# Kernel optimization log

Hardware: AMD Instinct MI355X
Metric: run time of the kernel (lower is better)

Reference implementation:

```python
import jax, jax.numpy as jnp
import numpy as np

# ---- module constants (from init_kwargs) ----
EMBED_DIM = 384
NUM_HYPEREDGES = 128
TOPK = 64
SPATIAL_SHAPE = (16, 32, 32)  # D, H, W -> N = 16384
SPACING = (2.0, 1.0, 1.0)
SPATIAL_WEIGHT = 0.1
B, N, C = 4, 16 * 32 * 32, EMBED_DIM


def _l2norm(x, axis=-1, eps=1e-12):
    n = jnp.linalg.norm(x, axis=axis, keepdims=True)
    return x / jnp.maximum(n, eps)


def _get_3d_coords():
    D, H, W = SPATIAL_SHAPE
    z = jnp.arange(D, dtype=jnp.float32) * SPACING[0]
    y = jnp.arange(H, dtype=jnp.float32) * SPACING[1]
    x = jnp.arange(W, dtype=jnp.float32) * SPACING[2]
    zz, yy, xx = jnp.meshgrid(z, y, x, indexing='ij')
    return jnp.stack([zz, yy, xx], axis=-1).reshape(-1, 3)  # (N, 3)


def setup_inputs() -> dict:
    key = jax.random.key(0)
    k1, k2 = jax.random.split(key)
    node_features = jax.random.normal(k1, (B, N, C), dtype=jnp.float32)
    class_token = jax.random.normal(k2, (1, 1, C), dtype=jnp.float32)
    temperature = jnp.ones((1,), dtype=jnp.float32) * 0.07
    return {"node_features": node_features, "class_token": class_token, "temperature": temperature}


def reference(node_features, class_token, temperature):
    Ne = NUM_HYPEREDGES
    w = SPATIAL_WEIGHT
    temp = temperature[0]

    nodes_n = _l2norm(node_features)                      # (B, N, C)

    # Step 1: center sampling by semantic similarity to class token
    ct_n = _l2norm(jnp.broadcast_to(class_token, (B, 1, C)))
    scores = jnp.einsum('boc,bnc->bn', ct_n, nodes_n) / temp  # (B, N)
    _, center_idx = jax.lax.top_k(scores, Ne)             # (B, Ne)

    # Gather centers and compute cosine sim of every center vs all nodes
    centers = jnp.take_along_axis(node_features, center_idx[:, :, None], axis=1)  # (B, Ne, C)
    centers_n = _l2norm(centers)
    sem_sim = jnp.einsum('bec,bnc->ben', centers_n, nodes_n) / temp  # (B, Ne, N)

    # Spatial bias (normalized distance from each center voxel)
    coords = _get_3d_coords()                             # (N, 3)
    center_coords = coords[center_idx]                    # (B, Ne, 3)
    diff = coords[None, None, :, :] - center_coords[:, :, None, :]  # (B, Ne, N, 3)
    dist = jnp.linalg.norm(diff, axis=-1)                 # (B, Ne, N)
    dist = dist / (jnp.max(dist, axis=-1, keepdims=True) + 1e-8)
    combined = (1.0 - w) * sem_sim + w * (1.0 - dist)     # (B, Ne, N)

    # Per-hyperedge top-K neighbors -> incidence matrix H (B, N, Ne)
    _, nbr_idx = jax.lax.top_k(combined, TOPK)            # (B, Ne, K)
    b_ix = jnp.arange(B)[:, None, None]
    e_ix = jnp.arange(Ne)[None, :, None]
    Hmat = jnp.zeros((B, N, Ne), dtype=node_features.dtype)
    Hmat = Hmat.at[b_ix, nbr_idx, e_ix].set(1.0)
    return Hmat
```

## Files before the change

### kernel.cpp

```cpp
#include <hip/hip_runtime.h>
#include <math.h>

#define BB 4
#define NN 16384
#define CC 384
#define NE 128
#define KK 64
#define CAP 1024

typedef unsigned short ushort_t;
typedef __attribute__((ext_vector_type(8))) short bf16x8;
typedef __attribute__((ext_vector_type(4))) float f32x4;
#define MFMA(a, b, c) __builtin_amdgcn_mfma_f32_16x16x32_bf16(a, b, c, 0, 0, 0)

__device__ inline unsigned fkey(float f) {
    unsigned b = __float_as_uint(f);
    return (b & 0x80000000u) ? ~b : (b | 0x80000000u);
}
__device__ inline ushort_t bf16rne(float f) {
    unsigned u = __float_as_uint(f);
    unsigned r = u + 0x7FFFu + ((u >> 16) & 1u);
    return (ushort_t)(r >> 16);
}
__device__ inline float bf16tof(ushort_t h) {
    return __uint_as_float(((unsigned)h) << 16);
}
__device__ inline void cvt2(float fa, float fb, unsigned& hp, unsigned& lp) {
    unsigned ua = __float_as_uint(fa), ub = __float_as_uint(fb);
    unsigned ra = ua + 0x8000u, rb = ub + 0x8000u;
    hp = (ra >> 16) | (rb & 0xFFFF0000u);
    float ha = __uint_as_float(ra & 0xFFFF0000u);
    float hb = __uint_as_float(rb & 0xFFFF0000u);
    float la = fa - ha, lb = fb - hb;
    unsigned lra = __float_as_uint(la) + 0x8000u;
    unsigned lrb = __float_as_uint(lb) + 0x8000u;
    lp = (lra >> 16) | (lrb & 0xFFFF0000u);
}

__device__ inline void bin_select4k(const unsigned* hist, int t, int* wsum,
                                    int* sh_bin, int* sh_r, int r) {
    int base = t * 4;
    int c0 = hist[base], c1 = hist[base + 1], c2 = hist[base + 2], c3 = hist[base + 3];
    int csum = c0 + c1 + c2 + c3;
    int lane = t & 63, wid = t >> 6;
    int x = csum;
#pragma unroll
    for (int off = 1; off < 64; off <<= 1) {
        int v = __shfl_down(x, off, 64);
        if (lane + off < 64) x += v;
    }
    if (lane == 0) wsum[wid] = x;
    __syncthreads();
    int after = 0;
    for (int w2 = wid + 1; w2 < 16; ++w2) after += wsum[w2];
    int S = x - csum + after;
    if (S < r && S + c3 >= r) { *sh_bin = base + 3; *sh_r = r - S; }
    S += c3;
    if (S < r && S + c2 >= r) { *sh_bin = base + 2; *sh_r = r - S; }
    S += c2;
    if (S < r && S + c1 >= r) { *sh_bin = base + 1; *sh_r = r - S; }
    S += c1;
    if (S < r && S + c0 >= r) { *sh_bin = base + 0; *sh_r = r - S; }
    __syncthreads();
}

__global__ __launch_bounds__(256) void k_scores(const float* __restrict__ nf,
                                                const float* __restrict__ ct,
                                                unsigned* __restrict__ keys,
                                                float* __restrict__ invn) {
    int wave = threadIdx.x >> 6;
    int lane = threadIdx.x & 63;
    int row  = blockIdx.x * 4 + wave;
    const float* x = nf + (size_t)row * CC;
    float4 a  = ((const float4*)x)[lane];
    float2 c2 = ((const float2*)(x + 256))[lane];
    float4 ta = ((const float4*)ct)[lane];
    float2 tc = ((const float2*)(ct + 256))[lane];
    float ss = a.x*a.x + a.y*a.y + a.z*a.z + a.w*a.w + c2.x*c2.x + c2.y*c2.y;
    float dt = ta.x*a.x + ta.y*a.y + ta.z*a.z + ta.w*a.w + tc.x*c2.x + tc.y*c2.y;
#pragma unroll
    for (int off = 32; off; off >>= 1) {
        ss += __shfl_xor(ss, off, 64);
        dt += __shfl_xor(dt, off, 64);
    }
    if (lane == 0) {
        float inv = 1.0f / fmaxf(sqrtf(ss), 1e-12f);
        invn[row] = inv;
        keys[row] = fkey(dt * inv);
    }
}

__global__ __launch_bounds__(1024) void k_top128(const unsigned* __restrict__ keys,
                                                 const float* __restrict__ nf,
                                                 const float* __restrict__ invn,
                                                 ushort_t* __restrict__ Ahi,
                                                 ushort_t* __restrict__ Alo,
                                                 float* __restrict__ meta) {
    __shared__ unsigned hist[4096];
    __shared__ int wsum[16];
    __shared__ int sh_bin, sh_r;
    __shared__ unsigned cu[NE];
    __shared__ int cil[NE];
    __shared__ unsigned eqk[CAP];
    __shared__ int eqi[CAP];
    __shared__ int cnt_gt, cnt_eq;
    __shared__ int ocid[NE];
    int b = blockIdx.x;
    int t = threadIdx.x;
    const uint4* rowv = (const uint4*)(keys + b * NN);
    if (t == 0) { cnt_gt = 0; cnt_eq = 0; }
    ((uint4*)hist)[t] = make_uint4(0, 0, 0, 0);
    __syncthreads();
    uint4 u0 = rowv[t], u1 = rowv[t + 1024], u2 = rowv[t + 2048], u3 = rowv[t + 3072];
    atomicAdd(&hist[u0.x >> 20], 1u); atomicAdd(&hist[u0.y >> 20], 1u);
    atomicAdd(&hist[u0.z >> 20], 1u); atomicAdd(&hist[u0.w >> 20], 1u);
    atomicAdd(&hist[u1.x >> 20], 1u); atomicAdd(&hist[u1.y >> 20], 1u);
    atomicAdd(&hist[u1.z >> 20], 1u); atomicAdd(&hist[u1.w >> 20], 1u);
    atomicAdd(&hist[u2.x >> 20], 1u); atomicAdd(&hist[u2.y >> 20], 1u);
    atomicAdd(&hist[u2.z >> 20], 1u); atomicAdd(&hist[u2.w >> 20], 1u);
    atomicAdd(&hist[u3.x >> 20], 1u); atomicAdd(&hist[u3.y >> 20], 1u);
    atomicAdd(&hist[u3.z >> 20], 1u); atomicAdd(&hist[u3.w >> 20], 1u);
    __syncthreads();
    bin_select4k(hist, t, wsum, &sh_bin, &sh_r, NE);
    unsigned bin = (unsigned)sh_bin;
    int r = sh_r;
#define EMIT128(uu, nn) { unsigned tb = (uu) >> 20; \
    if (tb > bin) { int p = atomicAdd(&cnt_gt, 1); cu[p] = (uu); cil[p] = (nn); } \
    else if (tb == bin) { int p = atomicAdd(&cnt_eq, 1); if (p < CAP) { eqk[p] = (uu); eqi[p] = (nn); } } }
    EMIT128(u0.x, 4*t+0); EMIT128(u0.y, 4*t+1); EMIT128(u0.z, 4*t+2); EMIT128(u0.w, 4*t+3);
    EMIT128(u1.x, 4096+4*t+0); EMIT128(u1.y, 4096+4*t+1); EMIT128(u1.z, 4096+4*t+2); EMIT128(u1.w, 4096+4*t+3);
    EMIT128(u2.x, 8192+4*t+0); EMIT128(u2.y, 8192+4*t+1); EMIT128(u2.z, 8192+4*t+2); EMIT128(u2.w, 8192+4*t+3);
    EMIT128(u3.x, 12288+4*t+0); EMIT128(u3.y, 12288+4*t+1); EMIT128(u3.z, 12288+4*t+2); EMIT128(u3.w, 12288+4*t+3);
#undef EMIT128
    __syncthreads();
    int ne = cnt_eq < CAP ? cnt_eq : CAP;
    for (int i = t; i < ne; i += 1024) {
        unsigned ki = eqk[i]; int ii = eqi[i], rk = 0;
        for (int j = 0; j < ne; ++j) {
            unsigned kj = eqk[j];
            rk += (kj > ki) || (kj == ki && eqi[j] < ii);
        }
        if (rk < r) { cu[cnt_gt + rk] = ki; cil[cnt_gt + rk] = ii; }
    }
    __syncthreads();
    if (t < NE) {
        unsigned mu = cu[t]; int mi = cil[t], rk = 0;
#pragma unroll 4
        for (int j = 0; j < NE; ++j) {
            unsigned ou = cu[j]; int oi = cil[j];
            rk += (ou > mu) || (ou == mu && oi < mi);
        }
        ocid[rk] = mi;
    }
    __syncthreads();
    {
        int e = t >> 3, part = t & 7;
        int ci = ocid[e];
        float inv = invn[b * NN + ci];
        const float4* src = (const float4*)(nf + ((size_t)b * NN + ci) * CC) + part * 12;
        ushort_t* dh = Ahi + ((size_t)b * NE + e) * CC + part * 48;
        ushort_t* dl = Alo + ((size_t)b * NE + e) * CC + part * 48;
#pragma unroll
        for (int i = 0; i < 12; ++i) {
            float4 f = src[i];
            f.x *= inv; f.y *= inv; f.z *= inv; f.w *= inv;
            ushort4 h, l;
            h.x = bf16rne(f.x); l.x = bf16rne(f.x - bf16tof(h.x));
            h.y = bf16rne(f.y); l.y = bf16rne(f.y - bf16tof(h.y));
            h.z = bf16rne(f.z); l.z = bf16rne(f.z - bf16tof(h.z));
            h.w = bf16rne(f.w); l.w = bf16rne(f.w - bf16tof(h.w));
            ((ushort4*)dh)[i] = h;
            ((ushort4*)dl)[i] = l;
        }
    }
    if (t < NE) {
        int ci = ocid[t];
        float zc = (float)(ci >> 10) * 2.0f;
        float yc = (float)((ci >> 5) & 31);
        float xc = (float)(ci & 31);
        float mz = fmaxf(zc * zc, (30.f - zc) * (30.f - zc));
        float my = fmaxf(yc * yc, (31.f - yc) * (31.f - yc));
        float mx = fmaxf(xc * xc, (31.f - xc) * (31.f - xc));
        float md = sqrtf(mz + my + mx);
        int be = b * NE + t;
        meta[be * 4 + 0] = zc;
        meta[be * 4 + 1] = yc;
        meta[be * 4 + 2] = xc;
        meta[be * 4 + 3] = 1.0f / (md + 1e-8f);
    }
}

__global__ __launch_bounds__(256, 4) void k_gemm(const float* __restrict__ nf,
                                                 const ushort_t* __restrict__ Ahi,
                                                 const ushort_t* __restrict__ Alo,
                                                 const float* __restrict__ invn,
                                                 const float* __restrict__ meta,
                                                 const float* __restrict__ temp,
                                                 unsigned* __restrict__ outk) {
    __shared__ ushort_t Ah[4][66][8], Al[4][66][8];
    __shared__ ushort_t Bh[4][130][8], Bl[4][130][8];
    __shared__ float ms[64 * 4];
    __shared__ float invs_s[128];
    int b  = blockIdx.y;
    int e0 = (blockIdx.x & 1) * 64;
    int n0 = (blockIdx.x >> 1) * 128;
    int t  = threadIdx.x;
    int w = t >> 6, lane = t & 63, quad = lane >> 4, mrow = lane & 15;
    int m0 = (w & 1) * 32, nw0 = (w >> 1) * 64;
    for (int i = t; i < 64 * 4; i += 256) ms[i] = meta[(b * NE + e0) * 4 + i];
    if (t < 128) invs_s[t] = invn[b * NN + n0 + t];
    f32x4 acc[2][4];
#pragma unroll
    for (int i = 0; i < 2; ++i)
#pragma unroll
        for (int j = 0; j < 4; ++j) acc[i][j] = (f32x4)0.f;
    const ushort_t* Abh = Ahi + ((size_t)b * NE + e0) * CC;
    const ushort_t* Abl = Alo + ((size_t)b * NE + e0) * CC;
    const float* Bb = nf + ((size_t)b * NN + n0) * CC;
    int ae = t >> 2, ak8 = t & 3;
    const ushort_t* agh = Abh + (size_t)ae * CC + ak8 * 8;
    const ushort_t* agl = Abl + (size_t)ae * CC + ak8 * 8;
    int bn0 = t >> 2, bk80 = t & 3;
    int bn1 = (t + 256) >> 2, bk81 = (t + 256) & 3;
    const float* bs0 = Bb + (size_t)bn0 * CC + bk80 * 8;
    const float* bs1 = Bb + (size_t)bn1 * CC + bk81 * 8;
    uint4 pAh, pAl;
    float4 pB0a, pB0b, pB1a, pB1b;
    pAh = *(const uint4*)agh;
    pAl = *(const uint4*)agl;
    pB0a = ((const float4*)bs0)[0]; pB0b = ((const float4*)bs0)[1];
    pB1a = ((const float4*)bs1)[0]; pB1b = ((const float4*)bs1)[1];
    for (int kt = 0; kt < CC; kt += 32) {
        __syncthreads();
        *(uint4*)&Ah[ak8][ae][0] = pAh;
        *(uint4*)&Al[ak8][ae][0] = pAl;
        {
            uint4 ph, pl;
            cvt2(pB0a.x, pB0a.y, ph.x, pl.x);
            cvt2(pB0a.z, pB0a.w, ph.y, pl.y);
            cvt2(pB0b.x, pB0b.y, ph.z, pl.z);
            cvt2(pB0b.z, pB0b.w, ph.w, pl.w);
            *(uint4*)&Bh[bk80][bn0][0] = ph;
            *(uint4*)&Bl[bk80][bn0][0] = pl;
            cvt2(pB1a.x, pB1a.y, ph.x, pl.x);
            cvt2(pB1a.z, pB1a.w, ph.y, pl.y);
            cvt2(pB1b.x, pB1b.y, ph.z, pl.z);
            cvt2(pB1b.z, pB1b.w, ph.w, pl.w);
            *(uint4*)&Bh[bk81][bn1][0] = ph;
            *(uint4*)&Bl[bk81][bn1][0] = pl;
        }
        if (kt + 32 < CC) {
            pAh = *(const uint4*)(agh + kt + 32);
            pAl = *(const uint4*)(agl + kt + 32);
            pB0a = ((const float4*)(bs0 + kt + 32))[0]; pB0b = ((const float4*)(bs0 + kt + 32))[1];
            pB1a = ((const float4*)(bs1 + kt + 32))[0]; pB1b = ((const float4*)(bs1 + kt + 32))[1];
        }
        __syncthreads();
        bf16x8 afh[2], afl[2], bfh[4], bfl[4];
#pragma unroll
        for (int i = 0; i < 2; ++i) {
            int m = m0 + i * 16 + mrow;
            afh[i] = *(const bf16x8*)&Ah[quad][m][0];
            afl[i] = *(const bf16x8*)&Al[quad][m][0];
        }
#pragma unroll
        for (int j = 0; j < 4; ++j) {
            int n = nw0 + j * 16 + mrow;
            bfh[j] = *(const bf16x8*)&Bh[quad][n][0];
            bfl[j] = *(const bf16x8*)&Bl[quad][n][0];
        }
#pragma unroll
        for (int i = 0; i < 2; ++i)
#pragma unroll
            for (int j = 0; j < 4; ++j) {
                acc[i][j] = MFMA(afh[i], bfh[j], acc[i][j]);
                acc[i][j] = MFMA(afh[i], bfl[j], acc[i][j]);
                acc[i][j] = MFMA(afl[i], bfh[j], acc[i][j]);
            }
    }
    float scale = 0.9f / temp[0];
#pragma unroll
    for (int j = 0; j < 4; ++j) {
        int nloc = nw0 + j * 16 + mrow;
        int n = n0 + nloc;
        float invnn = invs_s[nloc];
        float zf = (float)(n >> 10) * 2.0f;
        float yf = (float)((n >> 5) & 31);
        float xf = (float)(n & 31);
#pragma unroll
        for (int i = 0; i < 2; ++i) {
#pragma unroll
            for (int r = 0; r < 4; ++r) {
                int el = m0 + i * 16 + quad * 4 + r;
                float zc = ms[el * 4 + 0], yc = ms[el * 4 + 1], xc = ms[el * 4 + 2], ivd = ms[el * 4 + 3];
                float dz = zf - zc, dy = yf - yc, dx = xf - xc;
                float dist = sqrtf(dz * dz + dy * dy + dx * dx);
                float v = scale * invnn * acc[i][j][r] + 0.1f * (1.0f - dist * ivd);
                outk[((size_t)(b * NE + e0 + el)) * NN + n] = fkey(v);
            }
        }
    }
}

__global__ __launch_bounds__(1024) void k_top64(const unsigned* __restrict__ comb,
                                                int* __restrict__ sel) {
    __shared__ unsigned hist[4096];
    __shared__ int wsum[16];
    __shared__ int sh_bin, sh_r;
    __shared__ unsigned eqk[CAP];
    __shared__ int eqi[CAP];
    __shared__ int cnt_gt, cnt_eq;
    int be = blockIdx.x;
    int t  = threadIdx.x;
    const uint4* rowv = (const uint4*)(comb + (size_t)be * NN);
    if (t == 0) { cnt_gt = 0; cnt_eq = 0; }
    ((uint4*)hist)[t] = make_uint4(0, 0, 0, 0);
    __syncthreads();
    uint4 u0 = rowv[t], u1 = rowv[t + 1024], u2 = rowv[t + 2048], u3 = rowv[t + 3072];
    atomicAdd(&hist[u0.x >> 20], 1u); atomicAdd(&hist[u0.y >> 20], 1u);
    atomicAdd(&hist[u0.z >> 20], 1u); atomicAdd(&hist[u0.w >> 20], 1u);
    atomicAdd(&hist[u1.x >> 20], 1u); atomicAdd(&hist[u1.y >> 20], 1u);
    atomicAdd(&hist[u1.z >> 20], 1u); atomicAdd(&hist[u1.w >> 20], 1u);
    atomicAdd(&hist[u2.x >> 20], 1u); atomicAdd(&hist[u2.y >> 20], 1u);
    atomicAdd(&hist[u2.z >> 20], 1u); atomicAdd(&hist[u2.w >> 20], 1u);
    atomicAdd(&hist[u3.x >> 20], 1u); atomicAdd(&hist[u3.y >> 20], 1u);
    atomicAdd(&hist[u3.z >> 20], 1u); atomicAdd(&hist[u3.w >> 20], 1u);
    __syncthreads();
    bin_select4k(hist, t, wsum, &sh_bin, &sh_r, KK);
    unsigned bin = (unsigned)sh_bin;
    int r = sh_r;
#define EMIT64(uu, nn) { unsigned tb = (uu) >> 20; \
    if (tb > bin) { int p = atomicAdd(&cnt_gt, 1); sel[be * KK + p] = (nn); } \
    else if (tb == bin) { int p = atomicAdd(&cnt_eq, 1); if (p < CAP) { eqk[p] = (uu); eqi[p] = (nn); } } }
    EMIT64(u0.x, 4*t+0); EMIT64(u0.y, 4*t+1); EMIT64(u0.z, 4*t+2); EMIT64(u0.w, 4*t+3);
    EMIT64(u1.x, 4096+4*t+0); EMIT64(u1.y, 4096+4*t+1); EMIT64(u1.z, 4096+4*t+2); EMIT64(u1.w, 4096+4*t+3);
    EMIT64(u2.x, 8192+4*t+0); EMIT64(u2.y, 8192+4*t+1); EMIT64(u2.z, 8192+4*t+2); EMIT64(u2.w, 8192+4*t+3);
    EMIT64(u3.x, 12288+4*t+0); EMIT64(u3.y, 12288+4*t+1); EMIT64(u3.z, 12288+4*t+2); EMIT64(u3.w, 12288+4*t+3);
#undef EMIT64
    __syncthreads();
    int ne = cnt_eq < CAP ? cnt_eq : CAP;
    for (int i = t; i < ne; i += 1024) {
        unsigned ki = eqk[i]; int ii = eqi[i], rk = 0;
        for (int j = 0; j < ne; ++j) {
            unsigned kj = eqk[j];
            rk += (kj > ki) || (kj == ki && eqi[j] < ii);
        }
        if (rk < r) sel[be * KK + cnt_gt + rk] = ii;
    }
}

__global__ __launch_bounds__(256) void k_scatter(const int* __restrict__ sel,
                                                 float* __restrict__ H) {
    int gid = blockIdx.x * 256 + threadIdx.x;
    int b = gid >> 13;
    int e = (gid >> 6) & 127;
    int n = sel[gid];
    H[((size_t)b * NN + n) * NE + e] = 1.0f;
}

extern "C" void kernel_launch(void* const* d_in, const int* in_sizes, int n_in,
                              void* d_out, int out_size, void* d_ws, size_t ws_size,
                              hipStream_t stream) {
    const float* nf   = (const float*)d_in[0];
    const float* ct   = (const float*)d_in[1];
    const float* temp = (const float*)d_in[2];
    float* out = (float*)d_out;

    unsigned* keys = (unsigned*)d_ws;
    float* invn    = (float*)(keys + BB * NN);
    float* meta    = invn + BB * NN;
    ushort_t* Ahi  = (ushort_t*)(meta + BB * NE * 4);
    ushort_t* Alo  = Ahi + (size_t)BB * NE * CC;
    int* sel       = (int*)(Alo + (size_t)BB * NE * CC);

    k_scores <<<BB * NN / 4, 256, 0, stream>>>(nf, ct, keys, invn);
    k_top128 <<<BB, 1024, 0, stream>>>(keys, nf, invn, Ahi, Alo, meta);
    k_gemm   <<<dim3(NN / 128 * 2, BB), 256, 0, stream>>>(nf, Ahi, Alo, invn, meta, temp, (unsigned*)out);
    k_top64  <<<BB * NE, 1024, 0, stream>>>((const unsigned*)out, sel);
    hipMemsetAsync(d_out, 0, (size_t)BB * NN * NE * sizeof(float), stream);
    k_scatter<<<BB * NE * KK / 256, 256, 0, stream>>>(sel, out);
}
```

Baseline: 254.4 us.

## Replace memset+scatter with bitmask expand; split center packing; swizzle GEMM tiles

k_top64 now writes a per-hyperedge 16384-bit selection bitmask instead of an index list. A new k_expand kernel writes the full dense H output from that bitmask in one coalesced pass, which replaces the separate full-size memset followed by an uncoalesced scatter. Center normalization and bf16 hi/lo packing move out of the 4-block k_top128 into a separate 512-block k_centers kernel for more parallelism. The GEMM block index is remapped so neighbouring blocks share node tiles, which should improve cache reuse. The cost is one extra kernel launch and a small bitmask buffer in workspace.

Measured after the change: 236.5 us. -7.1%, faster.

```diff
diff --git a/kernel.cpp b/kernel.cpp
--- a/kernel.cpp
+++ b/kernel.cpp
@@ -91,10 +91,7 @@
 }
 
 __global__ __launch_bounds__(1024) void k_top128(const unsigned* __restrict__ keys,
-                                                 const float* __restrict__ nf,
-                                                 const float* __restrict__ invn,
-                                                 ushort_t* __restrict__ Ahi,
-                                                 ushort_t* __restrict__ Alo,
+                                                 int* __restrict__ cidx,
                                                  float* __restrict__ meta) {
     __shared__ unsigned hist[4096];
     __shared__ int wsum[16];
@@ -151,28 +148,9 @@
             rk += (ou > mu) || (ou == mu && oi < mi);
         }
         ocid[rk] = mi;
-    }
-    __syncthreads();
-    {
-        int e = t >> 3, part = t & 7;
-        int ci = ocid[e];
-        float inv = invn[b * NN + ci];
-        const float4* src = (const float4*)(nf + ((size_t)b * NN + ci) * CC) + part * 12;
-        ushort_t* dh = Ahi + ((size_t)b * NE + e) * CC + part * 48;
-        ushort_t* dl = Alo + ((size_t)b * NE + e) * CC + part * 48;
-#pragma unroll
-        for (int i = 0; i < 12; ++i) {
-            float4 f = src[i];
-            f.x *= inv; f.y *= inv; f.z *= inv; f.w *= inv;
-            ushort4 h, l;
-            h.x = bf16rne(f.x); l.x = bf16rne(f.x - bf16tof(h.x));
-            h.y = bf16rne(f.y); l.y = bf16rne(f.y - bf16tof(h.y));
-            h.z = bf16rne(f.z); l.z = bf16rne(f.z - bf16tof(h.z));
-            h.w = bf16rne(f.w); l.w = bf16rne(f.w - bf16tof(h.w));
-            ((ushort4*)dh)[i] = h;
-            ((ushort4*)dl)[i] = l;
-        }
-    }
+        cidx[b * NE + rk] = mi;
+    }
+    __syncthreads();
     if (t < NE) {
         int ci = ocid[t];
         float zc = (float)(ci >> 10) * 2.0f;
@@ -190,6 +168,36 @@
     }
 }
 
+__global__ __launch_bounds__(64) void k_centers(const float* __restrict__ nf,
+                                                const float* __restrict__ invn,
+                                                const int* __restrict__ cidx,
+                                                ushort_t* __restrict__ Ahi,
+                                                ushort_t* __restrict__ Alo) {
+    int be = blockIdx.x;
+    int b  = be >> 7;
+    int l  = threadIdx.x;
+    int ci = cidx[be];
+    float inv = invn[b * NN + ci];
+    const float* src = nf + ((size_t)b * NN + ci) * CC;
+    float4 a  = ((const float4*)src)[l];
+    float2 c2 = ((const float2*)(src + 256))[l];
+    a.x *= inv; a.y *= inv; a.z *= inv; a.w *= inv;
+    c2.x *= inv; c2.y *= inv;
+    ushort4 h4; ushort2 h2;
+    h4.x = bf16rne(a.x); h4.y = bf16rne(a.y); h4.z = bf16rne(a.z); h4.w = bf16rne(a.w);
+    h2.x = bf16rne(c2.x); h2.y = bf16rne(c2.y);
+    ushort4 l4; ushort2 l2;
+    l4.x = bf16rne(a.x - bf16tof(h4.x)); l4.y = bf16rne(a.y - bf16tof(h4.y));
+    l4.z = bf16rne(a.z - bf16tof(h4.z)); l4.w = bf16rne(a.w - bf16tof(h4.w));
+    l2.x = bf16rne(c2.x - bf16tof(h2.x)); l2.y = bf16rne(c2.y - bf16tof(h2.y));
+    ushort_t* dh = Ahi + (size_t)be * CC;
+    ushort_t* dl = Alo + (size_t)be * CC;
+    ((ushort4*)dh)[l] = h4;
+    ((ushort2*)(dh + 256))[l] = h2;
+    ((ushort4*)dl)[l] = l4;
+    ((ushort2*)(dl + 256))[l] = l2;
+}
+
 __global__ __launch_bounds__(256, 4) void k_gemm(const float* __restrict__ nf,
                                                  const ushort_t* __restrict__ Ahi,
                                                  const ushort_t* __restrict__ Alo,
@@ -202,8 +210,11 @@
     __shared__ float ms[64 * 4];
     __shared__ float invs_s[128];
     int b  = blockIdx.y;
-    int e0 = (blockIdx.x & 1) * 64;
-    int n0 = (blockIdx.x >> 1) * 128;
+    int x  = blockIdx.x;
+    int low = x & 15;
+    int e0 = (low >> 3) * 64;
+    int nt = (x >> 4) * 8 + (low & 7);
+    int n0 = nt * 128;
     int t  = threadIdx.x;
     int w = t >> 6, lane = t & 63, quad = lane >> 4, mrow = lane & 15;
     int m0 = (w & 1) * 32, nw0 = (w >> 1) * 64;
@@ -303,18 +314,20 @@
 }
 
 __global__ __launch_bounds__(1024) void k_top64(const unsigned* __restrict__ comb,
-                                                int* __restrict__ sel) {
+                                                unsigned* __restrict__ bmg) {
     __shared__ unsigned hist[4096];
+    __shared__ unsigned bm[512];
     __shared__ int wsum[16];
     __shared__ int sh_bin, sh_r;
     __shared__ unsigned eqk[CAP];
     __shared__ int eqi[CAP];
-    __shared__ int cnt_gt, cnt_eq;
+    __shared__ int cnt_eq;
     int be = blockIdx.x;
     int t  = threadIdx.x;
     const uint4* rowv = (const uint4*)(comb + (size_t)be * NN);
-    if (t == 0) { cnt_gt = 0; cnt_eq = 0; }
+    if (t == 0) cnt_eq = 0;
     ((uint4*)hist)[t] = make_uint4(0, 0, 0, 0);
+    if (t < 128) ((uint4*)bm)[t] = make_uint4(0, 0, 0, 0);
     __syncthreads();
     uint4 u0 = rowv[t], u1 = rowv[t + 1024], u2 = rowv[t + 2048], u3 = rowv[t + 3072];
     atomicAdd(&hist[u0.x >> 20], 1u); atomicAdd(&hist[u0.y >> 20], 1u);
@@ -330,7 +343,7 @@
     unsigned bin = (unsigned)sh_bin;
     int r = sh_r;
 #define EMIT64(uu, nn) { unsigned tb = (uu) >> 20; \
-    if (tb > bin) { int p = atomicAdd(&cnt_gt, 1); sel[be * KK + p] = (nn); } \
+    if (tb > bin) { atomicOr(&bm[(nn) >> 5], 1u << ((nn) & 31)); } \
     else if (tb == bin) { int p = atomicAdd(&cnt_eq, 1); if (p < CAP) { eqk[p] = (uu); eqi[p] = (nn); } } }
     EMIT64(u0.x, 4*t+0); EMIT64(u0.y, 4*t+1); EMIT64(u0.z, 4*t+2); EMIT64(u0.w, 4*t+3);
     EMIT64(u1.x, 4096+4*t+0); EMIT64(u1.y, 4096+4*t+1); EMIT64(u1.z, 4096+4*t+2); EMIT64(u1.w, 4096+4*t+3);
@@ -345,17 +358,35 @@
             unsigned kj = eqk[j];
             rk += (kj > ki) || (kj == ki && eqi[j] < ii);
         }
-        if (rk < r) sel[be * KK + cnt_gt + rk] = ii;
-    }
-}
-
-__global__ __launch_bounds__(256) void k_scatter(const int* __restrict__ sel,
-                                                 float* __restrict__ H) {
-    int gid = blockIdx.x * 256 + threadIdx.x;
-    int b = gid >> 13;
-    int e = (gid >> 6) & 127;
-    int n = sel[gid];
-    H[((size_t)b * NN + n) * NE + e] = 1.0f;
+        if (rk < r) atomicOr(&bm[ii >> 5], 1u << (ii & 31));
+    }
+    __syncthreads();
+    if (t < 128) ((uint4*)(bmg + (size_t)be * 512))[t] = ((uint4*)bm)[t];
+}
+
+__global__ __launch_bounds__(256) void k_expand(const unsigned* __restrict__ bmg,
+                                                float* __restrict__ H) {
+    __shared__ unsigned wl[256];
+    int b  = blockIdx.y;
+    int n0 = blockIdx.x * 64;
+    int t  = threadIdx.x;
+    int w0 = n0 >> 5;
+    wl[t] = bmg[((size_t)b * NE + (t >> 1)) * 512 + w0 + (t & 1)];
+    __syncthreads();
+    float4* dst = (float4*)(H + ((size_t)b * NN + n0) * NE);
+#pragma unroll
+    for (int i = 0; i < 8; ++i) {
+        int flat = t + 256 * i;
+        int nl = flat >> 5, f4 = flat & 31;
+        int wsel = nl >> 5, bit = nl & 31;
+        int e = f4 * 4;
+        float4 v;
+        v.x = (float)((wl[(e + 0) * 2 + wsel] >> bit) & 1u);
+        v.y = (float)((wl[(e + 1) * 2 + wsel] >> bit) & 1u);
+        v.z = (float)((wl[(e + 2) * 2 + wsel] >> bit) & 1u);
+        v.w = (float)((wl[(e + 3) * 2 + wsel] >> bit) & 1u);
+        dst[flat] = v;
+    }
 }
 
 extern "C" void kernel_launch(void* const* d_in, const int* in_sizes, int n_in,
@@ -371,12 +402,13 @@
     float* meta    = invn + BB * NN;
     ushort_t* Ahi  = (ushort_t*)(meta + BB * NE * 4);
     ushort_t* Alo  = Ahi + (size_t)BB * NE * CC;
-    int* sel       = (int*)(Alo + (size_t)BB * NE * CC);
+    int* cidx      = (int*)(Alo + (size_t)BB * NE * CC);
+    unsigned* bmg  = (unsigned*)(cidx + BB * NE);
 
     k_scores <<<BB * NN / 4, 256, 0, stream>>>(nf, ct, keys, invn);
-    k_top128 <<<BB, 1024, 0, stream>>>(keys, nf, invn, Ahi, Alo, meta);
+    k_top128 <<<BB, 1024, 0, stream>>>(keys, cidx, meta);
+    k_centers<<<BB * NE, 64, 0, stream>>>(nf, invn, cidx, Ahi, Alo);
     k_gemm   <<<dim3(NN / 128 * 2, BB), 256, 0, stream>>>(nf, Ahi, Alo, invn, meta, temp, (unsigned*)out);
-    k_top64  <<<BB * NE, 1024, 0, stream>>>((const unsigned*)out, sel);
-    hipMemsetAsync(d_out, 0, (size_t)BB * NN * NE * sizeof(float), stream);
-    k_scatter<<<BB * NE * KK / 256, 256, 0, stream>>>(sel, out);
-}
+    k_top64  <<<BB * NE, 1024, 0, stream>>>((const unsigned*)out, bmg);
+    k_expand <<<dim3(NN / 64, BB), 256, 0, stream>>>(bmg, out);
+}
```

## Store 16-bit combined keys, recompute ties exactly, emit incidence via bitmask expand

Applied to the files above, without the earlier changes.

The GEMM now writes only the upper 16 bits of each order-preserving key to a workspace buffer, which halves the intermediate traffic. The top-64 kernel selects on these truncated keys and recomputes exact fp32 scores only for candidates tied at the threshold. Selections go into a per-hyperedge bitmask, and a new expand kernel writes the dense H output directly, replacing the memset plus scatter. The GEMM block order is also remapped for locality. Tie handling relies on a 128-candidate cap, so rows with more ties could be wrong, and recomputed scores may differ slightly from the MFMA values.

New measurement: 240.7 us. 1.06x faster.

```diff
diff --git a/kernel.cpp b/kernel.cpp
--- a/kernel.cpp
+++ b/kernel.cpp
@@ -7,6 +7,7 @@
 #define NE 128
 #define KK 64
 #define CAP 1024
+#define CCAP 128
 
 typedef unsigned short ushort_t;
 typedef __attribute__((ext_vector_type(8))) short bf16x8;
@@ -196,14 +197,17 @@
                                                  const float* __restrict__ invn,
                                                  const float* __restrict__ meta,
                                                  const float* __restrict__ temp,
-                                                 unsigned* __restrict__ outk) {
+                                                 ushort_t* __restrict__ outk16) {
     __shared__ ushort_t Ah[4][66][8], Al[4][66][8];
     __shared__ ushort_t Bh[4][130][8], Bl[4][130][8];
     __shared__ float ms[64 * 4];
     __shared__ float invs_s[128];
     int b  = blockIdx.y;
-    int e0 = (blockIdx.x & 1) * 64;
-    int n0 = (blockIdx.x >> 1) * 128;
+    int x  = blockIdx.x;
+    int low = x & 15;
+    int e0 = (low >> 3) * 64;
+    int nt = (x >> 4) * 8 + (low & 7);
+    int n0 = nt * 128;
     int t  = threadIdx.x;
     int w = t >> 6, lane = t & 63, quad = lane >> 4, mrow = lane & 15;
     int m0 = (w & 1) * 32, nw0 = (w >> 1) * 64;
@@ -296,66 +300,146 @@
                 float dz = zf - zc, dy = yf - yc, dx = xf - xc;
                 float dist = sqrtf(dz * dz + dy * dy + dx * dx);
                 float v = scale * invnn * acc[i][j][r] + 0.1f * (1.0f - dist * ivd);
-                outk[((size_t)(b * NE + e0 + el)) * NN + n] = fkey(v);
+                outk16[((size_t)(b * NE + e0 + el)) * NN + n] = (ushort_t)(fkey(v) >> 16);
             }
         }
     }
 }
 
-__global__ __launch_bounds__(1024) void k_top64(const unsigned* __restrict__ comb,
-                                                int* __restrict__ sel) {
+__global__ __launch_bounds__(1024) void k_top64(const ushort_t* __restrict__ comb,
+                                                const float* __restrict__ nf,
+                                                const float* __restrict__ invn,
+                                                const ushort_t* __restrict__ Ahi,
+                                                const ushort_t* __restrict__ Alo,
+                                                const float* __restrict__ meta,
+                                                const float* __restrict__ temp,
+                                                unsigned* __restrict__ bmg) {
     __shared__ unsigned hist[4096];
+    __shared__ unsigned bm[512];
     __shared__ int wsum[16];
     __shared__ int sh_bin, sh_r;
     __shared__ unsigned eqk[CAP];
     __shared__ int eqi[CAP];
-    __shared__ int cnt_gt, cnt_eq;
+    __shared__ int cnt_eq, cnt_above, nc_sh;
+    __shared__ unsigned sh_T16;
+    __shared__ int candi[CCAP];
+    __shared__ float candv[CCAP];
     int be = blockIdx.x;
+    int b  = be >> 7;
     int t  = threadIdx.x;
     const uint4* rowv = (const uint4*)(comb + (size_t)be * NN);
-    if (t == 0) { cnt_gt = 0; cnt_eq = 0; }
+    if (t == 0) { cnt_eq = 0; cnt_above = 0; nc_sh = 0; }
     ((uint4*)hist)[t] = make_uint4(0, 0, 0, 0);
-    __syncthreads();
-    uint4 u0 = rowv[t], u1 = rowv[t + 1024], u2 = rowv[t + 2048], u3 = rowv[t + 3072];
-    atomicAdd(&hist[u0.x >> 20], 1u); atomicAdd(&hist[u0.y >> 20], 1u);
-    atomicAdd(&hist[u0.z >> 20], 1u); atomicAdd(&hist[u0.w >> 20], 1u);
-    atomicAdd(&hist[u1.x >> 20], 1u); atomicAdd(&hist[u1.y >> 20], 1u);
-    atomicAdd(&hist[u1.z >> 20], 1u); atomicAdd(&hist[u1.w >> 20], 1u);
-    atomicAdd(&hist[u2.x >> 20], 1u); atomicAdd(&hist[u2.y >> 20], 1u);
-    atomicAdd(&hist[u2.z >> 20], 1u); atomicAdd(&hist[u2.w >> 20], 1u);
-    atomicAdd(&hist[u3.x >> 20], 1u); atomicAdd(&hist[u3.y >> 20], 1u);
-    atomicAdd(&hist[u3.z >> 20], 1u); atomicAdd(&hist[u3.w >> 20], 1u);
+    if (t < 128) ((uint4*)bm)[t] = make_uint4(0, 0, 0, 0);
+    __syncthreads();
+    uint4 u0 = rowv[t], u1 = rowv[t + 1024];
+    unsigned ks[16]; int ns[16];
+    ks[0] = u0.x & 0xFFFFu; ks[1] = u0.x >> 16; ks[2] = u0.y & 0xFFFFu; ks[3] = u0.y >> 16;
+    ks[4] = u0.z & 0xFFFFu; ks[5] = u0.z >> 16; ks[6] = u0.w & 0xFFFFu; ks[7] = u0.w >> 16;
+    ks[8]  = u1.x & 0xFFFFu; ks[9]  = u1.x >> 16; ks[10] = u1.y & 0xFFFFu; ks[11] = u1.y >> 16;
+    ks[12] = u1.z & 0xFFFFu; ks[13] = u1.z >> 16; ks[14] = u1.w & 0xFFFFu; ks[15] = u1.w >> 16;
+#pragma unroll
+    for (int j = 0; j < 8; ++j) { ns[j] = 8 * t + j; ns[8 + j] = 8192 + 8 * t + j; }
+#pragma unroll
+    for (int j = 0; j < 16; ++j) atomicAdd(&hist[ks[j] >> 4], 1u);
     __syncthreads();
     bin_select4k(hist, t, wsum, &sh_bin, &sh_r, KK);
-    unsigned bin = (unsigned)sh_bin;
+    unsigned b12 = (unsigned)sh_bin;
     int r = sh_r;
-#define EMIT64(uu, nn) { unsigned tb = (uu) >> 20; \
-    if (tb > bin) { int p = atomicAdd(&cnt_gt, 1); sel[be * KK + p] = (nn); } \
-    else if (tb == bin) { int p = atomicAdd(&cnt_eq, 1); if (p < CAP) { eqk[p] = (uu); eqi[p] = (nn); } } }
-    EMIT64(u0.x, 4*t+0); EMIT64(u0.y, 4*t+1); EMIT64(u0.z, 4*t+2); EMIT64(u0.w, 4*t+3);
-    EMIT64(u1.x, 4096+4*t+0); EMIT64(u1.y, 4096+4*t+1); EMIT64(u1.z, 4096+4*t+2); EMIT64(u1.w, 4096+4*t+3);
-    EMIT64(u2.x, 8192+4*t+0); EMIT64(u2.y, 8192+4*t+1); EMIT64(u2.z, 8192+4*t+2); EMIT64(u2.w, 8192+4*t+3);
-    EMIT64(u3.x, 12288+4*t+0); EMIT64(u3.y, 12288+4*t+1); EMIT64(u3.z, 12288+4*t+2); EMIT64(u3.w, 12288+4*t+3);
-#undef EMIT64
+#pragma unroll
+    for (int j = 0; j < 16; ++j) {
+        unsigned bj = ks[j] >> 4;
+        if (bj > b12) {
+            atomicOr(&bm[ns[j] >> 5], 1u << (ns[j] & 31));
+        } else if (bj == b12) {
+            int p = atomicAdd(&cnt_eq, 1);
+            if (p < CAP) { eqk[p] = ks[j]; eqi[p] = ns[j]; }
+        }
+    }
     __syncthreads();
     int ne = cnt_eq < CAP ? cnt_eq : CAP;
-    for (int i = t; i < ne; i += 1024) {
-        unsigned ki = eqk[i]; int ii = eqi[i], rk = 0;
-        for (int j = 0; j < ne; ++j) {
-            unsigned kj = eqk[j];
-            rk += (kj > ki) || (kj == ki && eqi[j] < ii);
-        }
-        if (rk < r) sel[be * KK + cnt_gt + rk] = ii;
-    }
-}
-
-__global__ __launch_bounds__(256) void k_scatter(const int* __restrict__ sel,
-                                                 float* __restrict__ H) {
-    int gid = blockIdx.x * 256 + threadIdx.x;
-    int b = gid >> 13;
-    int e = (gid >> 6) & 127;
-    int n = sel[gid];
-    H[((size_t)b * NN + n) * NE + e] = 1.0f;
+    if (t < ne) {
+        unsigned ki = eqk[t]; int gt = 0, eq = 0;
+        for (int j = 0; j < ne; ++j) { unsigned kj = eqk[j]; gt += (kj > ki); eq += (kj == ki); }
+        if (gt < r && gt + eq >= r) sh_T16 = ki;
+    }
+    __syncthreads();
+    unsigned T16 = sh_T16;
+    if (t < ne) {
+        unsigned ki = eqk[t];
+        if (ki > T16) {
+            atomicAdd(&cnt_above, 1);
+            atomicOr(&bm[eqi[t] >> 5], 1u << (eqi[t] & 31));
+        } else if (ki == T16) {
+            int p = atomicAdd(&nc_sh, 1);
+            if (p < CCAP) candi[p] = eqi[t];
+        }
+    }
+    __syncthreads();
+    int r2 = r - cnt_above;
+    int nc = nc_sh < CCAP ? nc_sh : CCAP;
+    int wid = t >> 6, lane = t & 63;
+    float scale = 0.9f / temp[0];
+    for (int c = wid; c < nc; c += 16) {
+        int n = candi[c];
+        const float* xr = nf + ((size_t)b * NN + n) * CC;
+        const ushort_t* ch = Ahi + (size_t)be * CC;
+        const ushort_t* cl = Alo + (size_t)be * CC;
+        float s = 0.f;
+#pragma unroll
+        for (int j = 0; j < 6; ++j) {
+            int cc = lane + 64 * j;
+            float cv = bf16tof(ch[cc]) + bf16tof(cl[cc]);
+            s += cv * xr[cc];
+        }
+#pragma unroll
+        for (int off = 32; off; off >>= 1) s += __shfl_xor(s, off, 64);
+        if (lane == 0) {
+            float zc = meta[be * 4 + 0], yc = meta[be * 4 + 1], xc = meta[be * 4 + 2], ivd = meta[be * 4 + 3];
+            float zf = (float)(n >> 10) * 2.0f;
+            float yf = (float)((n >> 5) & 31);
+            float xf = (float)(n & 31);
+            float dz = zf - zc, dy = yf - yc, dx = xf - xc;
+            float dist = sqrtf(dz * dz + dy * dy + dx * dx);
+            candv[c] = scale * invn[b * NN + n] * s + 0.1f * (1.0f - dist * ivd);
+        }
+    }
+    __syncthreads();
+    if (t < nc) {
+        float vi = candv[t]; int ii = candi[t], rk = 0;
+        for (int j = 0; j < nc; ++j) {
+            float vj = candv[j];
+            rk += (vj > vi) || (vj == vi && candi[j] < ii);
+        }
+        if (rk < r2) atomicOr(&bm[ii >> 5], 1u << (ii & 31));
+    }
+    __syncthreads();
+    if (t < 128) ((uint4*)(bmg + (size_t)be * 512))[t] = ((uint4*)bm)[t];
+}
+
+__global__ __launch_bounds__(256) void k_expand(const unsigned* __restrict__ bmg,
+                                                float* __restrict__ H) {
+    __shared__ unsigned wl[256];
+    int b  = blockIdx.y;
+    int n0 = blockIdx.x * 64;
+    int t  = threadIdx.x;
+    int w0 = n0 >> 5;
+    wl[t] = bmg[((size_t)b * NE + (t >> 1)) * 512 + w0 + (t & 1)];
+    __syncthreads();
+    float4* dst = (float4*)(H + ((size_t)b * NN + n0) * NE);
+#pragma unroll
+    for (int i = 0; i < 8; ++i) {
+        int flat = t + 256 * i;
+        int nl = flat >> 5, f4 = flat & 31;
+        int wsel = nl >> 5, bit = nl & 31;
+        int e = f4 * 4;
+        float4 v;
+        v.x = (float)((wl[(e + 0) * 2 + wsel] >> bit) & 1u);
+        v.y = (float)((wl[(e + 1) * 2 + wsel] >> bit) & 1u);
+        v.z = (float)((wl[(e + 2) * 2 + wsel] >> bit) & 1u);
+        v.w = (float)((wl[(e + 3) * 2 + wsel] >> bit) & 1u);
+        dst[flat] = v;
+    }
 }
 
 extern "C" void kernel_launch(void* const* d_in, const int* in_sizes, int n_in,
@@ -371,12 +455,12 @@
     float* meta    = invn + BB * NN;
     ushort_t* Ahi  = (ushort_t*)(meta + BB * NE * 4);
     ushort_t* Alo  = Ahi + (size_t)BB * NE * CC;
-    int* sel       = (int*)(Alo + (size_t)BB * NE * CC);
+    unsigned* bmg  = (unsigned*)(Alo + (size_t)BB * NE * CC);
+    ushort_t* k16  = (ushort_t*)(bmg + (size_t)BB * NE * 512);
 
     k_scores <<<BB * NN / 4, 256, 0, stream>>>(nf, ct, keys, invn);
     k_top128 <<<BB, 1024, 0, stream>>>(keys, nf, invn, Ahi, Alo, meta);
-    k_gemm   <<<dim3(NN / 128 * 2, BB), 256, 0, stream>>>(nf, Ahi, Alo, invn, meta, temp, (unsigned*)out);
-    k_top64  <<<BB * NE, 1024, 0, stream>>>((const unsigned*)out, sel);
-    hipMemsetAsync(d_out, 0, (size_t)BB * NN * NE * sizeof(float), stream);
-    k_scatter<<<BB * NE * KK / 256, 256, 0, stream>>>(sel, out);
-}
+    k_gemm   <<<dim3(NN / 128 * 2, BB), 256, 0, stream>>>(nf, Ahi, Alo, invn, meta, temp, k16);
+    k_top64  <<<BB * NE, 1024, 0, stream>>>(k16, nf, invn, Ahi, Alo, meta, temp, bmg);
+    k_expand <<<dim3(NN / 64, BB), 256, 0, stream>>>(bmg, out);
+}
```
